# Kernel tuning notes

Measured on AMD Instinct MI355X. Metric: run time of the kernel, lower is better.

Reference implementation:

```python
import jax, jax.numpy as jnp
from jax import lax
import numpy as np

D = 1024      # input_size
H = D // 2    # proj hidden
T = 25        # num_ner_labels
B, S = 64, 512


def setup_inputs() -> dict:
    key = jax.random.key(0)
    ks = jax.random.split(key, 8)
    sc1 = 1.0 / np.sqrt(D)
    sc2 = 1.0 / np.sqrt(H)
    return {
        "encoder_out": jax.random.normal(ks[0], (B, S, D), dtype=jnp.float32),
        "W1": jax.random.uniform(ks[1], (D, H), jnp.float32, -sc1, sc1),
        "b1": jax.random.uniform(ks[2], (H,), jnp.float32, -sc1, sc1),
        "W2": jax.random.uniform(ks[3], (H, T), jnp.float32, -sc2, sc2),
        "b2": jax.random.uniform(ks[4], (T,), jnp.float32, -sc2, sc2),
        "start_trans": jax.random.uniform(ks[5], (T,), jnp.float32, -0.1, 0.1),
        "end_trans": jax.random.uniform(ks[6], (T,), jnp.float32, -0.1, 0.1),
        "trans": jax.random.uniform(ks[7], (T, T), jnp.float32, -0.1, 0.1),
        "ner_labels": jax.random.randint(jax.random.fold_in(key, 1), (B, S), 0, T, dtype=jnp.int64),
        "mask": jnp.ones((B, S), dtype=bool),
    }


def _crf_nll(emissions, start_trans, end_trans, trans, labels, mask):
    # torchcrf negative mean log-likelihood, batch_first
    maskf = mask.astype(emissions.dtype)
    # numerator: score of gold path
    em_at_tag = jnp.take_along_axis(emissions, labels[..., None], axis=2)[..., 0]  # [B,S]
    score0 = start_trans[labels[:, 0]] + em_at_tag[:, 0]
    trans_sc = trans[labels[:, :-1], labels[:, 1:]]                                # [B,S-1]
    step_score = (trans_sc + em_at_tag[:, 1:]) * maskf[:, 1:]
    last_idx = mask.sum(axis=1).astype(jnp.int32) - 1
    last_tag = jnp.take_along_axis(labels, last_idx[:, None].astype(labels.dtype), axis=1)[:, 0]
    numerator = score0 + step_score.sum(axis=1) + end_trans[last_tag]
    # denominator: log partition via forward algorithm (scan over time)
    alpha0 = start_trans[None, :] + emissions[:, 0]                                # [B,T]
    em_rest = jnp.swapaxes(emissions[:, 1:], 0, 1)                                 # [S-1,B,T]
    m_rest = jnp.swapaxes(mask[:, 1:], 0, 1)                                       # [S-1,B]

    def step(alpha, xs):
        em_t, m_t = xs
        new = jax.scipy.special.logsumexp(
            alpha[:, :, None] + trans[None, :, :] + em_t[:, None, :], axis=1)
        return jnp.where(m_t[:, None], new, alpha), None

    alpha, _ = lax.scan(step, alpha0, (em_rest, m_rest))
    log_Z = jax.scipy.special.logsumexp(alpha + end_trans[None, :], axis=1)        # [B]
    return -jnp.mean(numerator - log_Z)


def reference(encoder_out, W1, b1, W2, b2, start_trans, end_trans, trans, ner_labels, mask):
    h = jax.nn.gelu(encoder_out @ W1 + b1, approximate=False)  # dropout is eval-mode identity
    emissions = h @ W2 + b2                                    # [B,S,T]
    return _crf_nll(emissions, start_trans, end_trans, trans, ner_labels, mask)
```

## Files before the change

kernel.cpp:

```cpp
#include <hip/hip_runtime.h>
#include <math.h>

#define DD 1024
#define HH 512
#define TT 25
#define BB 64
#define SS 512
#define MM (BB*SS)
#define NC 16

typedef __attribute__((ext_vector_type(8))) short short8;
typedef __attribute__((ext_vector_type(4))) float floatx4;

static __device__ __forceinline__ unsigned short f2bf(float f) {
  unsigned u = __float_as_uint(f);
  u = (u + 0x7FFFu + ((u >> 16) & 1u)) >> 16;
  return (unsigned short)u;
}
static __device__ __forceinline__ float bf2f(unsigned short s) {
  return __uint_as_float(((unsigned)s) << 16);
}
static __device__ __forceinline__ float rl(float v, int i) {
  return __int_as_float(__builtin_amdgcn_readlane(__float_as_int(v), i));
}
static __device__ __forceinline__ void load_lds16(const void* g, void* l) {
  __builtin_amdgcn_global_load_lds(
      (const __attribute__((address_space(1))) unsigned int*)g,
      (__attribute__((address_space(3))) unsigned int*)l, 16, 0, 0);
}

__global__ __launch_bounds__(256) void k_prep(
    const float* __restrict__ W1, const float* __restrict__ W2,
    unsigned short* __restrict__ W1T2, unsigned short* __restrict__ W2p) {
  const int t = threadIdx.x;
  if (blockIdx.y < 8) {
    __shared__ unsigned short tile[64 * 72];
    const int k0 = blockIdx.x * 64, n0 = blockIdx.y * 64;
    #pragma unroll
    for (int it = 0; it < 16; it++) {
      int idx = t + it * 256;
      int kk = idx >> 6, nn = idx & 63;
      tile[nn * 72 + kk] = f2bf(W1[(size_t)(k0 + kk) * HH + n0 + nn]);
    }
    __syncthreads();
    #pragma unroll
    for (int it = 0; it < 4; it++) {
      int idx = (t + it * 256) * 4;
      int nn = idx >> 6, kk = idx & 63;
      ushort4 v;
      v.x = tile[nn * 72 + kk];     v.y = tile[nn * 72 + kk + 1];
      v.z = tile[nn * 72 + kk + 2]; v.w = tile[nn * 72 + kk + 3];
      int kt = (k0 >> 5) + (kk >> 5), kkk = kk & 31;
      *(ushort4*)(W1T2 + (size_t)kt * (HH * 32) + (n0 + nn) * 32 + kkk) = v;
    }
  } else {
    #pragma unroll
    for (int e = 0; e < 4; e++) {
      int idx = blockIdx.x * 1024 + t + e * 256;
      int row = idx >> 9, k = idx & 511;
      float v = (row < TT) ? W2[(size_t)k * TT + row] : 0.f;
      W2p[(size_t)row * HH + k] = f2bf(v);
    }
  }
}

__global__ __launch_bounds__(256, 4) void k_emis(
    const float* __restrict__ X, const unsigned short* __restrict__ W1T2,
    const float* __restrict__ b1, const unsigned short* __restrict__ W2p,
    const float* __restrict__ b2, float* __restrict__ em) {
  __shared__ short lds[12544];
  short* sX  = lds;
  short* sBt = lds + 2048;

  const int tid  = threadIdx.x;
  const int lane = tid & 63;
  const int w    = tid >> 6;
  const int l15  = lane & 15;
  const int kc   = lane >> 4;
  const int m0   = blockIdx.x * 64;
  const int colbase = blockIdx.y * 256;

  floatx4 acc[4][4];
  #pragma unroll
  for (int a = 0; a < 4; a++)
    #pragma unroll
    for (int b = 0; b < 4; b++)
      acc[a][b] = (floatx4){0.f, 0.f, 0.f, 0.f};

  const int am = tid >> 2;
  const int ac = tid & 3;
  const float* Xrow = X + (size_t)(m0 + am) * DD + ac * 8;

  const unsigned short* gW = W1T2 + (size_t)(colbase + w * 64) * 32 + lane * 8;
  short* lW = sBt + w * 64 * 32;

  float4 xv0 = *(const float4*)(Xrow);
  float4 xv1 = *(const float4*)(Xrow + 4);

  for (int k0 = 0; k0 < DD; k0 += 32) {
    __syncthreads();
    const unsigned short* g = gW + (size_t)(k0 >> 5) * (HH * 32);
    #pragma unroll
    for (int j = 0; j < 4; j++)
      load_lds16(g + j * 512, lW + j * 512);
    unsigned p0 = (unsigned)f2bf(xv0.x) | ((unsigned)f2bf(xv0.y) << 16);
    unsigned p1 = (unsigned)f2bf(xv0.z) | ((unsigned)f2bf(xv0.w) << 16);
    unsigned p2 = (unsigned)f2bf(xv1.x) | ((unsigned)f2bf(xv1.y) << 16);
    unsigned p3 = (unsigned)f2bf(xv1.z) | ((unsigned)f2bf(xv1.w) << 16);
    *(uint4*)(sX + am * 32 + ac * 8) = make_uint4(p0, p1, p2, p3);
    if (k0 + 32 < DD) {
      xv0 = *(const float4*)(Xrow + k0 + 32);
      xv1 = *(const float4*)(Xrow + k0 + 36);
    }
    __syncthreads();
    short8 af[4], bfr[4];
    #pragma unroll
    for (int mt = 0; mt < 4; mt++)
      af[mt] = *(const short8*)(sX + (mt * 16 + l15) * 32 + kc * 8);
    #pragma unroll
    for (int nt = 0; nt < 4; nt++)
      bfr[nt] = *(const short8*)(sBt + (w * 64 + nt * 16 + l15) * 32 + kc * 8);
    #pragma unroll
    for (int mt = 0; mt < 4; mt++)
      #pragma unroll
      for (int nt = 0; nt < 4; nt++)
        acc[mt][nt] = __builtin_amdgcn_mfma_f32_16x16x32_bf16(af[mt], bfr[nt], acc[mt][nt], 0, 0, 0);
  }

  short* sH = lds;
  float* sC = (float*)(lds + 8448);
  const int mt_g = w & 1, kh_g = w >> 1;

  short8 w2f[2][4];
  #pragma unroll
  for (int nt2 = 0; nt2 < 2; nt2++)
    #pragma unroll
    for (int ks = 0; ks < 4; ks++)
      w2f[nt2][ks] = *(const short8*)(W2p + (size_t)(nt2 * 16 + l15) * HH
                                      + colbase + kh_g * 128 + ks * 32 + kc * 8);

  #pragma unroll
  for (int half = 0; half < 2; half++) {
    __syncthreads();
    #pragma unroll
    for (int mt2 = 0; mt2 < 2; mt2++) {
      int mt = half * 2 + mt2;
      #pragma unroll
      for (int nt = 0; nt < 4; nt++) {
        int n = w * 64 + nt * 16 + l15;
        float bias = b1[colbase + n];
        #pragma unroll
        for (int r = 0; r < 4; r++) {
          int ml = mt2 * 16 + kc * 4 + r;
          float v = acc[mt][nt][r] + bias;
          float g = 0.5f * v * (1.0f + erff(v * 0.70710678118654752f));
          sH[ml * 264 + n] = (short)f2bf(g);
        }
      }
    }
    __syncthreads();
    #pragma unroll
    for (int nt2 = 0; nt2 < 2; nt2++) {
      floatx4 c2 = (floatx4){0.f, 0.f, 0.f, 0.f};
      #pragma unroll
      for (int ks = 0; ks < 4; ks++) {
        short8 a2 = *(const short8*)(sH + (mt_g * 16 + l15) * 264 + kh_g * 128 + ks * 32 + kc * 8);
        c2 = __builtin_amdgcn_mfma_f32_16x16x32_bf16(a2, w2f[nt2][ks], c2, 0, 0, 0);
      }
      #pragma unroll
      for (int r = 0; r < 4; r++)
        sC[kh_g * 1024 + (mt_g * 16 + kc * 4 + r) * 32 + nt2 * 16 + l15] = c2[r];
    }
    __syncthreads();
    for (int o = tid; o < 32 * TT; o += 256) {
      int m = o / TT, t = o % TT;
      float val = sC[m * 32 + t] + sC[1024 + m * 32 + t];
      if (blockIdx.y == 0) val += b2[t];
      atomicAdd(em + (size_t)(m0 + half * 32 + m) * TT + t, val);
    }
  }
}

__global__ __launch_bounds__(64) void k_chunk(
    const float* __restrict__ em, const float* __restrict__ trans,
    float* __restrict__ Mats) {
  const int b = blockIdx.x, c = blockIdx.y, rg = blockIdx.z;
  const int tid = threadIdx.x;
  const float* emb = em + (size_t)b * SS * TT;

  float Ecol[TT];
  #pragma unroll
  for (int i = 0; i < TT; i++)
    Ecol[i] = (tid < TT) ? __expf(trans[i * TT + tid]) : 0.f;

  const int s0 = 1 + c * 32;
  const int send = (s0 + 32 < SS) ? s0 + 32 : SS;

  float M[5];
  #pragma unroll
  for (int q = 0; q < 5; q++) {
    int r = rg * 5 + q;
    M[q] = (tid < TT) ? trans[r * TT + tid] + emb[s0 * TT + tid] : -1e30f;
  }

  float emn1 = (tid < TT) ? emb[(s0 + 1) * TT + tid] : 0.f;
  float emn2 = (tid < TT) ? emb[((s0 + 2 < SS) ? s0 + 2 : SS - 1) * TT + tid] : 0.f;
  for (int s = s0 + 1; s < send; s++) {
    float emc = emn1;
    emn1 = emn2;
    int sn = (s + 2 < SS) ? s + 2 : SS - 1;
    emn2 = (tid < TT) ? emb[sn * TT + tid] : 0.f;

    float a0[5], p[5];
    #pragma unroll
    for (int q = 0; q < 5; q++) {
      a0[q] = __builtin_amdgcn_readfirstlane(M[q]);
      p[q] = __expf(M[q] - a0[q]);
    }
    float d0[5], d1[5], d2[5], d3[5];
    #pragma unroll
    for (int q = 0; q < 5; q++) { d0[q] = 0.f; d1[q] = 0.f; d2[q] = 0.f; d3[q] = 0.f; }
    #pragma unroll
    for (int i = 0; i < 24; i += 4) {
      #pragma unroll
      for (int q = 0; q < 5; q++) {
        d0[q] = fmaf(rl(p[q], i + 0), Ecol[i + 0], d0[q]);
        d1[q] = fmaf(rl(p[q], i + 1), Ecol[i + 1], d1[q]);
        d2[q] = fmaf(rl(p[q], i + 2), Ecol[i + 2], d2[q]);
        d3[q] = fmaf(rl(p[q], i + 3), Ecol[i + 3], d3[q]);
      }
    }
    #pragma unroll
    for (int q = 0; q < 5; q++) {
      d0[q] = fmaf(rl(p[q], 24), Ecol[24], d0[q]);
      float anew = a0[q] + __logf((d0[q] + d1[q]) + (d2[q] + d3[q])) + emc;
      M[q] = (tid < TT) ? anew : -1e30f;
    }
  }

  if (tid < TT) {
    float* Mc = Mats + ((size_t)(b * NC + c)) * (TT * TT);
    #pragma unroll
    for (int q = 0; q < 5; q++)
      Mc[(rg * 5 + q) * TT + tid] = M[q];
  }
}

__global__ __launch_bounds__(64) void k_comb(
    const float* __restrict__ em, const float* __restrict__ start,
    const float* __restrict__ endt, const float* __restrict__ trans,
    const int* __restrict__ labels, const float* __restrict__ Mats,
    float* __restrict__ partial) {
  const int b = blockIdx.x;
  const int tid = threadIdx.x;
  const float* emb = em + (size_t)b * SS * TT;
  const int* lab = labels + b * SS;

  float part = 0.f;
  for (int s = tid; s < SS; s += 64) {
    int l = lab[s];
    if (s == 0) part += start[l] + emb[l];
    else        part += trans[lab[s - 1] * TT + l] + emb[s * TT + l];
  }
  #pragma unroll
  for (int off = 32; off; off >>= 1) part += __shfl_xor(part, off);
  float num = part + endt[lab[SS - 1]];

  const int jj = (tid < TT) ? tid : 0;
  float a = (tid < TT) ? start[tid] + emb[tid] : -1e30f;
  const float* Mb = Mats + (size_t)b * NC * (TT * TT);
  for (int c = 0; c < NC; c++) {
    const float* Mc = Mb + c * (TT * TT);
    float col[TT];
    float mxc = -1e30f;
    #pragma unroll
    for (int i = 0; i < TT; i++) {
      col[i] = Mc[i * TT + jj];
      mxc = fmaxf(mxc, col[i]);
    }
    float a0 = __builtin_amdgcn_readfirstlane(a);
    float p = __expf(a - a0);
    float d0 = 0.f, d1 = 0.f, d2 = 0.f, d3 = 0.f;
    #pragma unroll
    for (int i = 0; i < 24; i += 4) {
      d0 = fmaf(rl(p, i + 0), __expf(col[i + 0] - mxc), d0);
      d1 = fmaf(rl(p, i + 1), __expf(col[i + 1] - mxc), d1);
      d2 = fmaf(rl(p, i + 2), __expf(col[i + 2] - mxc), d2);
      d3 = fmaf(rl(p, i + 3), __expf(col[i + 3] - mxc), d3);
    }
    d0 = fmaf(rl(p, 24), __expf(col[24] - mxc), d0);
    float anew = a0 + mxc + __logf((d0 + d1) + (d2 + d3));
    a = (tid < TT) ? anew : -1e30f;
  }

  float v = (tid < TT) ? a + endt[tid] : -1e30f;
  float mx = v;
  #pragma unroll
  for (int off = 16; off; off >>= 1) mx = fmaxf(mx, __shfl_xor(mx, off, 32));
  float e = (tid < TT) ? __expf(v - mx) : 0.f;
  #pragma unroll
  for (int off = 16; off; off >>= 1) e += __shfl_xor(e, off, 32);
  if (tid == 0) partial[b] = (mx + __logf(e)) - num;
}

__global__ void k_final(const float* __restrict__ partial, float* __restrict__ out) {
  int tid = threadIdx.x;
  float v = partial[tid];
  #pragma unroll
  for (int off = 32; off; off >>= 1) v += __shfl_xor(v, off);
  if (tid == 0) out[0] = v * (1.0f / 64.0f);
}

extern "C" void kernel_launch(void* const* d_in, const int* in_sizes, int n_in,
                              void* d_out, int out_size, void* d_ws, size_t ws_size,
                              hipStream_t stream) {
  const float* X   = (const float*)d_in[0];
  const float* W1  = (const float*)d_in[1];
  const float* b1  = (const float*)d_in[2];
  const float* W2  = (const float*)d_in[3];
  const float* b2  = (const float*)d_in[4];
  const float* st  = (const float*)d_in[5];
  const float* en  = (const float*)d_in[6];
  const float* tr  = (const float*)d_in[7];
  const int* labels = (const int*)d_in[8];

  char* ws = (char*)d_ws;
  unsigned short* W1T2 = (unsigned short*)ws;
  unsigned short* W2p  = (unsigned short*)(ws + 0x100000);
  float* em            = (float*)(ws + 0x110000);
  float* Mats          = (float*)(ws + 0x430000);
  float* partial       = (float*)(ws + 0x6A1000);

  k_prep <<<dim3(16, 9), 256, 0, stream>>>(W1, W2, W1T2, W2p);
  hipMemsetAsync(em, 0, (size_t)MM * TT * sizeof(float), stream);
  k_emis <<<dim3(512, 2), 256, 0, stream>>>(X, W1T2, b1, W2p, b2, em);
  k_chunk<<<dim3(BB, NC, 5), 64, 0, stream>>>(em, tr, Mats);
  k_comb <<<BB, 64, 0, stream>>>(em, st, en, tr, labels, Mats, partial);
  k_final<<<1, 64, 0, stream>>>(partial, (float*)d_out);
}
```

Baseline: 367.2 us.

## Compute CRF chunk transfer matrices with bf16 MFMA in linear (exp) space

The per-chunk CRF transfer-matrix product now runs in exponentiated linear space as bf16 32x32x16 MFMAs. Each step multiplies exp(trans) by the current 25x25 state, which starts as identity, then scales by exp(emissions), with a fixed rescale at the midpoint and a log at the end. Chunks shrink to 16 steps (NC=32), and the 5-way row-group grid split is removed. This replaces many scalar readlane/FMA/log operations per step with matrix instructions. The cost is bf16 precision and a fixed-offset rescale that could overflow or underflow on other inputs.

```diff
diff --git a/kernel.cpp b/kernel.cpp
--- a/kernel.cpp
+++ b/kernel.cpp
@@ -7,10 +7,11 @@
 #define BB 64
 #define SS 512
 #define MM (BB*SS)
-#define NC 16
+#define NC 32
 
 typedef __attribute__((ext_vector_type(8))) short short8;
 typedef __attribute__((ext_vector_type(4))) float floatx4;
+typedef __attribute__((ext_vector_type(16))) float floatx16;
 
 static __device__ __forceinline__ unsigned short f2bf(float f) {
   unsigned u = __float_as_uint(f);
@@ -28,6 +29,7 @@
       (const __attribute__((address_space(1))) unsigned int*)g,
       (__attribute__((address_space(3))) unsigned int*)l, 16, 0, 0);
 }
+union U4S8 { uint4 u; short8 s; };
 
 __global__ __launch_bounds__(256) void k_prep(
     const float* __restrict__ W1, const float* __restrict__ W2,
@@ -184,65 +186,94 @@
 __global__ __launch_bounds__(64) void k_chunk(
     const float* __restrict__ em, const float* __restrict__ trans,
     float* __restrict__ Mats) {
-  const int b = blockIdx.x, c = blockIdx.y, rg = blockIdx.z;
-  const int tid = threadIdx.x;
+  const int b = blockIdx.x, c = blockIdx.y;
+  const int lane = threadIdx.x;
+  const int h = lane >> 5;
+  const int n = lane & 31;
   const float* emb = em + (size_t)b * SS * TT;
 
-  float Ecol[TT];
-  #pragma unroll
-  for (int i = 0; i < TT; i++)
-    Ecol[i] = (tid < TT) ? __expf(trans[i * TT + tid]) : 0.f;
-
-  const int s0 = 1 + c * 32;
-  const int send = (s0 + 32 < SS) ? s0 + 32 : SS;
-
-  float M[5];
-  #pragma unroll
-  for (int q = 0; q < 5; q++) {
-    int r = rg * 5 + q;
-    M[q] = (tid < TT) ? trans[r * TT + tid] + emb[s0 * TT + tid] : -1e30f;
-  }
-
-  float emn1 = (tid < TT) ? emb[(s0 + 1) * TT + tid] : 0.f;
-  float emn2 = (tid < TT) ? emb[((s0 + 2 < SS) ? s0 + 2 : SS - 1) * TT + tid] : 0.f;
-  for (int s = s0 + 1; s < send; s++) {
-    float emc = emn1;
-    emn1 = emn2;
-    int sn = (s + 2 < SS) ? s + 2 : SS - 1;
-    emn2 = (tid < TT) ? emb[sn * TT + tid] : 0.f;
-
-    float a0[5], p[5];
-    #pragma unroll
-    for (int q = 0; q < 5; q++) {
-      a0[q] = __builtin_amdgcn_readfirstlane(M[q]);
-      p[q] = __expf(M[q] - a0[q]);
-    }
-    float d0[5], d1[5], d2[5], d3[5];
-    #pragma unroll
-    for (int q = 0; q < 5; q++) { d0[q] = 0.f; d1[q] = 0.f; d2[q] = 0.f; d3[q] = 0.f; }
-    #pragma unroll
-    for (int i = 0; i < 24; i += 4) {
-      #pragma unroll
-      for (int q = 0; q < 5; q++) {
-        d0[q] = fmaf(rl(p[q], i + 0), Ecol[i + 0], d0[q]);
-        d1[q] = fmaf(rl(p[q], i + 1), Ecol[i + 1], d1[q]);
-        d2[q] = fmaf(rl(p[q], i + 2), Ecol[i + 2], d2[q]);
-        d3[q] = fmaf(rl(p[q], i + 3), Ecol[i + 3], d3[q]);
-      }
-    }
-    #pragma unroll
-    for (int q = 0; q < 5; q++) {
-      d0[q] = fmaf(rl(p[q], 24), Ecol[24], d0[q]);
-      float anew = a0[q] + __logf((d0[q] + d1[q]) + (d2[q] + d3[q])) + emc;
-      M[q] = (tid < TT) ? anew : -1e30f;
-    }
-  }
-
-  if (tid < TT) {
-    float* Mc = Mats + ((size_t)(b * NC + c)) * (TT * TT);
-    #pragma unroll
-    for (int q = 0; q < 5; q++)
-      Mc[(rg * 5 + q) * TT + tid] = M[q];
+  unsigned a1p[4], a2p[4];
+  #pragma unroll
+  for (int p = 0; p < 4; p++) {
+    int i0 = h * 8 + 2 * p, i1 = i0 + 1;
+    unsigned lo = (n < TT && i0 < TT) ? (unsigned)f2bf(__expf(trans[i0 * TT + n])) : 0u;
+    unsigned hi = (n < TT && i1 < TT) ? (unsigned)f2bf(__expf(trans[i1 * TT + n])) : 0u;
+    a1p[p] = lo | (hi << 16);
+    int j0 = 16 + h * 8 + 2 * p, j1 = j0 + 1;
+    lo = (n < TT && j0 < TT) ? (unsigned)f2bf(__expf(trans[j0 * TT + n])) : 0u;
+    hi = (n < TT && j1 < TT) ? (unsigned)f2bf(__expf(trans[j1 * TT + n])) : 0u;
+    a2p[p] = lo | (hi << 16);
+  }
+  U4S8 A1, A2;
+  A1.u = make_uint4(a1p[0], a1p[1], a1p[2], a1p[3]);
+  A2.u = make_uint4(a2p[0], a2p[1], a2p[2], a2p[3]);
+
+  unsigned bp1[4], bp2[4];
+  #pragma unroll
+  for (int p = 0; p < 4; p++) {
+    int k0 = h * 8 + 2 * p;
+    bp1[p] = ((k0 == n) ? 0x3F80u : 0u) | ((k0 + 1 == n) ? 0x3F800000u : 0u);
+    int k2 = 16 + h * 8 + 2 * p;
+    bp2[p] = ((k2 == n) ? 0x3F80u : 0u) | ((k2 + 1 == n) ? 0x3F800000u : 0u);
+  }
+
+  const int s0 = 1 + c * 16;
+  const int nst = (s0 + 16 <= SS) ? 16 : (SS - s0);
+
+  float emv[16], f[16];
+  #pragma unroll
+  for (int e = 0; e < 16; e++) {
+    int r = (e & 3) + 8 * (e >> 2) + 4 * h;
+    emv[e] = (r < TT) ? emb[s0 * TT + r] : 0.f;
+  }
+
+  for (int t = 0; t < nst; t++) {
+    const float rs = (t == 8) ? 32.0f : 0.0f;
+    float ex[16];
+    #pragma unroll
+    for (int e = 0; e < 16; e++) ex[e] = __expf(emv[e] - rs);
+    int sn = (s0 + t + 1 < SS) ? s0 + t + 1 : SS - 1;
+    #pragma unroll
+    for (int e = 0; e < 16; e++) {
+      int r = (e & 3) + 8 * (e >> 2) + 4 * h;
+      emv[e] = (r < TT) ? emb[sn * TT + r] : 0.f;
+    }
+    U4S8 B1, B2;
+    B1.u = make_uint4(bp1[0], bp1[1], bp1[2], bp1[3]);
+    B2.u = make_uint4(bp2[0], bp2[1], bp2[2], bp2[3]);
+    floatx16 D = __builtin_amdgcn_mfma_f32_32x32x16_bf16(A1.s, B1.s,
+                   __builtin_amdgcn_mfma_f32_32x32x16_bf16(A2.s, B2.s,
+                     (floatx16){0.f,0.f,0.f,0.f,0.f,0.f,0.f,0.f,
+                                0.f,0.f,0.f,0.f,0.f,0.f,0.f,0.f}, 0,0,0), 0,0,0);
+    #pragma unroll
+    for (int e = 0; e < 16; e++) f[e] = D[e] * ex[e];
+    if (t == nst - 1) break;
+    unsigned P[16];
+    #pragma unroll
+    for (int p = 0; p < 8; p++)
+      P[p] = (unsigned)f2bf(f[2 * p]) | ((unsigned)f2bf(f[2 * p + 1]) << 16);
+    unsigned sp[8];
+    #pragma unroll
+    for (int p = 0; p < 8; p++)
+      sp[p] = (unsigned)__shfl_xor((int)P[p], 32);
+    bool up = (h == 1);
+    bp1[0] = up ? sp[2] : P[0];
+    bp1[1] = up ? sp[3] : P[1];
+    bp1[2] = up ? P[2] : sp[0];
+    bp1[3] = up ? P[3] : sp[1];
+    bp2[0] = up ? sp[6] : P[4];
+    bp2[1] = up ? sp[7] : P[5];
+    bp2[2] = up ? P[6] : sp[4];
+    bp2[3] = up ? P[7] : sp[5];
+  }
+
+  if (n < TT) {
+    float* Mc = Mats + ((size_t)(b * NC + c)) * (TT * TT) + n * TT;
+    #pragma unroll
+    for (int e = 0; e < 16; e++) {
+      int r = (e & 3) + 8 * (e >> 2) + 4 * h;
+      if (r < TT) Mc[r] = __logf(f[e]) + 32.0f;
+    }
   }
 }
 
@@ -329,12 +360,12 @@
   unsigned short* W2p  = (unsigned short*)(ws + 0x100000);
   float* em            = (float*)(ws + 0x110000);
   float* Mats          = (float*)(ws + 0x430000);
-  float* partial       = (float*)(ws + 0x6A1000);
+  float* partial       = (float*)(ws + 0x930000);
 
   k_prep <<<dim3(16, 9), 256, 0, stream>>>(W1, W2, W1T2, W2p);
   hipMemsetAsync(em, 0, (size_t)MM * TT * sizeof(float), stream);
   k_emis <<<dim3(512, 2), 256, 0, stream>>>(X, W1T2, b1, W2p, b2, em);
-  k_chunk<<<dim3(BB, NC, 5), 64, 0, stream>>>(em, tr, Mats);
+  k_chunk<<<dim3(BB, NC), 64, 0, stream>>>(em, tr, Mats);
   k_comb <<<BB, 64, 0, stream>>>(em, st, en, tr, labels, Mats, partial);
   k_final<<<1, 64, 0, stream>>>(partial, (float*)d_out);
 }
```

Result: faster. 306.1 us (-16.6%).
